# Kernel tuning notes

Measured on AMD Instinct MI355X. Metric: run time of the kernel, lower is better.

Reference implementation:

```python
import jax, jax.numpy as jnp
import numpy as np

HEADS = 4
DIM_HEAD = 32
SCALE = DIM_HEAD ** -0.5


def setup_inputs() -> dict:
    key = jax.random.key(0)
    k1, k2, k3 = jax.random.split(key, 3)
    dim, hidden = 256, HEADS * DIM_HEAD
    x = jax.random.normal(k1, (4, dim, 64, 64), dtype=jnp.float32)
    w_qkv = jax.random.normal(k2, (hidden * 3, dim), dtype=jnp.float32) * (dim ** -0.5)
    w_out = jax.random.normal(k3, (dim, hidden), dtype=jnp.float32) * (hidden ** -0.5)
    b_out = jnp.zeros((dim,), dtype=jnp.float32)
    return {"x": x, "w_qkv": w_qkv, "w_out": w_out, "b_out": b_out}


def reference(x, w_qkv, w_out, b_out):
    b, c, h, w = x.shape
    # 1x1 conv (no bias) == channel matmul
    qkv = jnp.einsum('bchw,oc->bohw', x, w_qkv)           # [b, 3*hidden, h, w]
    q, k, v = jnp.split(qkv, 3, axis=1)
    def to_heads(t):
        # [b, heads*d, h, w] -> [b, heads, h*w, d]
        return t.reshape(b, HEADS, DIM_HEAD, h * w).transpose(0, 1, 3, 2)
    q, k, v = to_heads(q) * SCALE, to_heads(k), to_heads(v)
    sim = jnp.einsum('bhid,bhjd->bhij', q, k)             # [b, heads, hw, hw]
    attn = jax.nn.softmax(sim, axis=-1)
    out = jnp.einsum('bhij,bhjd->bhid', attn, v)          # [b, heads, hw, d]
    out = out.transpose(0, 1, 3, 2).reshape(b, HEADS * DIM_HEAD, h, w)
    # output 1x1 conv with bias
    return jnp.einsum('bchw,oc->bohw', out, w_out) + b_out[None, :, None, None]
```

## Files before the change

kernel.cpp:

```cpp
#include <hip/hip_runtime.h>
#include <hip/hip_fp16.h>

#define HEADS 4
#define DH    32
#define HW    4096
#define CIN   256
#define HID   128

using half8   = __attribute__((ext_vector_type(8))) _Float16;
using half4   = __attribute__((ext_vector_type(4))) _Float16;
using floatx4 = __attribute__((ext_vector_type(4))) float;

#define SHIFT2 4.328085122666891f
#define WQSCALE 0.25508275947f

__global__ __launch_bounds__(256) void qkv_fused(
    const float* __restrict__ w, const float* __restrict__ x,
    _Float16* __restrict__ Qw, _Float16* __restrict__ Kw,
    _Float16* __restrict__ Vtw)
{
  __shared__ float t[64][65];
  __shared__ _Float16 As[64][72];
  __shared__ _Float16 Bs[64][72];
  const int mt = blockIdx.x, nt = blockIdx.y;
  const int b = nt >> 6, p0 = (nt & 63) * 64;
  const int tid = threadIdx.x;
  const int wv = tid >> 6, lane = tid & 63, lm = lane & 15, quad = lane >> 4;
  const float wscale = (mt < 2) ? WQSCALE : 1.0f;

  const float* Ag = w + (size_t)(mt * 64) * CIN;
  const float* xb = x + (size_t)b * CIN * HW + p0;

  floatx4 acc[4] = {{0,0,0,0},{0,0,0,0},{0,0,0,0},{0,0,0,0}};

  for (int kq = 0; kq < 4; ++kq) {
    __syncthreads();
    #pragma unroll
    for (int i = 0; i < 4; ++i) {
      int ci = tid + i * 256;
      int cc = ci >> 4, p4 = (ci & 15) * 4;
      *(float4*)&t[cc][p4] =
          *(const float4*)(xb + (size_t)(kq * 64 + cc) * HW + p4);
    }
    #pragma unroll
    for (int i = 0; i < 2; ++i) {
      int ci = tid + i * 256;
      int r = ci >> 3, c8 = (ci & 7) * 8;
      const float* src = Ag + (size_t)r * CIN + kq * 64 + c8;
      float4 u0 = *(const float4*)(src);
      float4 u1 = *(const float4*)(src + 4);
      half8 h = {(_Float16)(u0.x * wscale), (_Float16)(u0.y * wscale),
                 (_Float16)(u0.z * wscale), (_Float16)(u0.w * wscale),
                 (_Float16)(u1.x * wscale), (_Float16)(u1.y * wscale),
                 (_Float16)(u1.z * wscale), (_Float16)(u1.w * wscale)};
      *(half8*)&As[r][c8] = h;
    }
    __syncthreads();
    #pragma unroll
    for (int i = 0; i < 2; ++i) {
      int idx = tid + i * 256;
      int p = idx >> 3, c0 = (idx & 7) * 8;
      half8 v;
      #pragma unroll
      for (int k = 0; k < 8; ++k) v[k] = (_Float16)t[c0 + k][p];
      *(half8*)&Bs[p][c0] = v;
    }
    __syncthreads();
    #pragma unroll
    for (int ks = 0; ks < 2; ++ks) {
      half8 a = *(const half8*)&As[wv * 16 + lm][ks * 32 + quad * 8];
      #pragma unroll
      for (int ns = 0; ns < 4; ++ns) {
        half8 bf = *(const half8*)&Bs[ns * 16 + lm][ks * 32 + quad * 8];
        acc[ns] = __builtin_amdgcn_mfma_f32_16x16x32_f16(a, bf, acc[ns], 0, 0, 0);
      }
    }
  }

  const int sec = mt >> 1;
  const int o_base = (mt & 1) * 64 + wv * 16 + quad * 4;
  const int hh = o_base >> 5, dd = o_base & 31;
  const int bh = b * HEADS + hh;
  if (sec < 2) {
    _Float16* dst = (sec == 0) ? Qw : Kw;
    #pragma unroll
    for (int ns = 0; ns < 4; ++ns) {
      int p = p0 + ns * 16 + lm;
      half4 v = {(_Float16)acc[ns][0], (_Float16)acc[ns][1],
                 (_Float16)acc[ns][2], (_Float16)acc[ns][3]};
      *(half4*)(dst + ((size_t)bh * HW + p) * DH + dd) = v;
    }
  } else {
    #pragma unroll
    for (int ns = 0; ns < 4; ++ns) {
      int p = p0 + ns * 16 + lm;
      #pragma unroll
      for (int r = 0; r < 4; ++r)
        Vtw[((size_t)bh * DH + dd + r) * HW + p] = (_Float16)acc[ns][r];
    }
  }
}

__global__ __launch_bounds__(256) void attn(
    const _Float16* __restrict__ Qw, const _Float16* __restrict__ Kw,
    const _Float16* __restrict__ Vtw, _Float16* __restrict__ Ot)
{
  __shared__ _Float16 ks[2][2][64][40];
  __shared__ _Float16 vt[2][2][32][72];

  const int bh = blockIdx.y, qt = blockIdx.x;
  const int tid = threadIdx.x;
  const int wv = tid >> 6, lane = tid & 63, lm = lane & 15, quad = lane >> 4;

  const _Float16* qptr = Qw + ((size_t)bh * HW + qt * 64 + wv * 16 + lm) * DH + quad * 8;
  const half8 qa = *(const half8*)qptr;

  const _Float16 one = (_Float16)1.0f;
  const half4 ones4 = {one, one, one, one};
  const floatx4 shiftc = {-SHIFT2, -SHIFT2, -SHIFT2, -SHIFT2};

  floatx4 oT[2] = {{0,0,0,0},{0,0,0,0}};
  floatx4 l4    = {0,0,0,0};

  const _Float16* kbase = Kw  + (size_t)bh * HW * DH;
  const _Float16* vbase = Vtw + (size_t)bh * DH * HW;
  const int kr = tid >> 2, kc = (tid & 3) * 8;
  const int vr = tid >> 3, vc = (tid & 7) * 8;

  half8 kA = *(const half8*)(kbase + (size_t)kr * DH + kc);
  half8 vA = *(const half8*)(vbase + (size_t)vr * HW + vc);
  half8 kB = *(const half8*)(kbase + ((size_t)64 + kr) * DH + kc);
  half8 vB = *(const half8*)(vbase + (size_t)vr * HW + 64 + vc);
  *(half8*)&ks[0][0][kr][kc] = kA;
  *(half8*)&vt[0][0][vr][vc] = vA;
  *(half8*)&ks[0][1][kr][kc] = kB;
  *(half8*)&vt[0][1][vr][vc] = vB;
  kA = *(const half8*)(kbase + ((size_t)128 + kr) * DH + kc);
  vA = *(const half8*)(vbase + (size_t)vr * HW + 128 + vc);
  kB = *(const half8*)(kbase + ((size_t)192 + kr) * DH + kc);
  vB = *(const half8*)(vbase + (size_t)vr * HW + 192 + vc);
  __syncthreads();

  for (int it = 0; it < HW / 128; ++it) {
    const int ph = it & 1, nx = ph ^ 1;
    *(half8*)&ks[nx][0][kr][kc] = kA;
    *(half8*)&vt[nx][0][vr][vc] = vA;
    *(half8*)&ks[nx][1][kr][kc] = kB;
    *(half8*)&vt[nx][1][vr][vc] = vB;
    const size_t koff = (size_t)(it * 2 + 4) * 64;
    kA = *(const half8*)(kbase + (koff + kr) * DH + kc);
    vA = *(const half8*)(vbase + (size_t)vr * HW + koff + vc);
    kB = *(const half8*)(kbase + (koff + 64 + kr) * DH + kc);
    vB = *(const half8*)(vbase + (size_t)vr * HW + koff + 64 + vc);

    #pragma unroll
    for (int sub = 0; sub < 2; ++sub) {
      floatx4 sT[4];
      #pragma unroll
      for (int f = 0; f < 4; ++f) {
        half8 kb = *(const half8*)&ks[ph][sub][f * 16 + lm][quad * 8];
        sT[f] = __builtin_amdgcn_mfma_f32_16x16x32_f16(kb, qa, shiftc, 0, 0, 0);
      }
      #pragma unroll
      for (int f = 0; f < 4; ++f) {
        half4 pb;
        #pragma unroll
        for (int r = 0; r < 4; ++r)
          pb[r] = (_Float16)__builtin_amdgcn_exp2f(sT[f][r]);
        l4 = __builtin_amdgcn_mfma_f32_16x16x16f16(ones4, pb, l4, 0, 0, 0);
        #pragma unroll
        for (int g = 0; g < 2; ++g) {
          half4 va = *(const half4*)&vt[ph][sub][g * 16 + lm][f * 16 + quad * 4];
          oT[g] = __builtin_amdgcn_mfma_f32_16x16x16f16(va, pb, oT[g], 0, 0, 0);
        }
      }
    }
    __syncthreads();
  }

  const float inv = 1.0f / l4[0];
  const int b = bh >> 2, hh = bh & 3;
  _Float16* obase = Ot + ((size_t)(b * HW + qt * 64 + wv * 16 + lm)) * HID + hh * DH;
  #pragma unroll
  for (int g = 0; g < 2; ++g) {
    half4 v = {(_Float16)(oT[g][0] * inv), (_Float16)(oT[g][1] * inv),
               (_Float16)(oT[g][2] * inv), (_Float16)(oT[g][3] * inv)};
    *(half4*)(obase + g * 16 + quad * 4) = v;
  }
}

__global__ __launch_bounds__(256) void out_gemm(
    const float* __restrict__ wo, const _Float16* __restrict__ Ot,
    const float* __restrict__ bo, float* __restrict__ out)
{
  __shared__ _Float16 As[64][136];
  __shared__ _Float16 Bs[64][136];
  __shared__ float os[64][68];
  const int mt = blockIdx.x, nt = blockIdx.y;
  const int b = nt >> 6, p0 = (nt & 63) * 64;
  const int tid = threadIdx.x;
  const int wv = tid >> 6, lane = tid & 63, lm = lane & 15, quad = lane >> 4;

  const float* Ag = wo + (size_t)(mt * 64) * HID;
  const _Float16* B = Ot + ((size_t)b * HW + p0) * HID;

  #pragma unroll
  for (int i = 0; i < 4; ++i) {
    int ci = tid + i * 256;
    int r = ci >> 4, c8 = (ci & 15) * 8;
    const float* src = Ag + (size_t)r * HID + c8;
    float4 u0 = *(const float4*)(src);
    float4 u1 = *(const float4*)(src + 4);
    half8 h = {(_Float16)u0.x, (_Float16)u0.y, (_Float16)u0.z, (_Float16)u0.w,
               (_Float16)u1.x, (_Float16)u1.y, (_Float16)u1.z, (_Float16)u1.w};
    *(half8*)&As[r][c8] = h;
    *(half8*)&Bs[r][c8] = *(const half8*)(B + (size_t)r * HID + c8);
  }
  __syncthreads();

  floatx4 acc[4] = {{0,0,0,0},{0,0,0,0},{0,0,0,0},{0,0,0,0}};
  #pragma unroll
  for (int ks = 0; ks < 4; ++ks) {
    half8 a = *(const half8*)&As[wv * 16 + lm][ks * 32 + quad * 8];
    #pragma unroll
    for (int ns = 0; ns < 4; ++ns) {
      half8 bf = *(const half8*)&Bs[ns * 16 + lm][ks * 32 + quad * 8];
      acc[ns] = __builtin_amdgcn_mfma_f32_16x16x32_f16(a, bf, acc[ns], 0, 0, 0);
    }
  }

  #pragma unroll
  for (int ns = 0; ns < 4; ++ns)
    #pragma unroll
    for (int r = 0; r < 4; ++r)
      os[wv * 16 + quad * 4 + r][ns * 16 + lm] = acc[ns][r];
  __syncthreads();

  const int o = tid >> 2, pq = (tid & 3) * 16;
  const float bias = bo[mt * 64 + o];
  float* dst = out + ((size_t)(b * CIN + mt * 64 + o)) * HW + p0 + pq;
  #pragma unroll
  for (int j = 0; j < 4; ++j) {
    float4 v = *(const float4*)&os[o][pq + j * 4];
    v.x += bias; v.y += bias; v.z += bias; v.w += bias;
    *(float4*)(dst + j * 4) = v;
  }
}

extern "C" void kernel_launch(void* const* d_in, const int* in_sizes, int n_in,
                              void* d_out, int out_size, void* d_ws, size_t ws_size,
                              hipStream_t stream)
{
  const float* x     = (const float*)d_in[0];
  const float* w_qkv = (const float*)d_in[1];
  const float* w_out = (const float*)d_in[2];
  const float* b_out = (const float*)d_in[3];
  float* out = (float*)d_out;

  char* ws = (char*)d_ws;
  _Float16* Ot  = (_Float16*)(ws);
  _Float16* Qw  = (_Float16*)(ws + (8u  << 20));
  _Float16* Kw  = (_Float16*)(ws + (12u << 20));
  _Float16* Vtw = (_Float16*)(ws + (16u << 20));

  dim3 blk(256);
  qkv_fused<<<dim3(6, 256), blk, 0, stream>>>(w_qkv, x, Qw, Kw, Vtw);
  attn<<<dim3(64, 16), blk, 0, stream>>>(Qw, Kw, Vtw, Ot);
  out_gemm<<<dim3(4, 256), blk, 0, stream>>>(w_out, Ot, b_out, out);
}
```

Measured before the change: 165.4 us.

## Process two query tiles per attention block to reuse staged K/V tiles

```diff
diff --git a/kernel.cpp b/kernel.cpp
--- a/kernel.cpp
+++ b/kernel.cpp
@@ -9,10 +9,15 @@
 
 using half8   = __attribute__((ext_vector_type(8))) _Float16;
 using half4   = __attribute__((ext_vector_type(4))) _Float16;
+using half2v  = __attribute__((ext_vector_type(2))) _Float16;
 using floatx4 = __attribute__((ext_vector_type(4))) float;
 
 #define SHIFT2 4.328085122666891f
 #define WQSCALE 0.25508275947f
+
+static __device__ __forceinline__ half2v pk2(float a, float b) {
+  return __builtin_bit_cast(half2v, __builtin_amdgcn_cvt_pkrtz(a, b));
+}
 
 __global__ __launch_bounds__(256) void qkv_fused(
     const float* __restrict__ w, const float* __restrict__ x,
@@ -106,21 +111,23 @@
     const _Float16* __restrict__ Vtw, _Float16* __restrict__ Ot)
 {
   __shared__ _Float16 ks[2][2][64][40];
-  __shared__ _Float16 vt[2][2][32][72];
+  __shared__ _Float16 vt[2][2][32][74];
 
   const int bh = blockIdx.y, qt = blockIdx.x;
   const int tid = threadIdx.x;
   const int wv = tid >> 6, lane = tid & 63, lm = lane & 15, quad = lane >> 4;
 
-  const _Float16* qptr = Qw + ((size_t)bh * HW + qt * 64 + wv * 16 + lm) * DH + quad * 8;
-  const half8 qa = *(const half8*)qptr;
+  const _Float16* qbase =
+      Qw + ((size_t)bh * HW + qt * 128 + wv * 16 + lm) * DH + quad * 8;
+  const half8 qa0 = *(const half8*)qbase;
+  const half8 qa1 = *(const half8*)(qbase + (size_t)64 * DH);
 
   const _Float16 one = (_Float16)1.0f;
   const half4 ones4 = {one, one, one, one};
   const floatx4 shiftc = {-SHIFT2, -SHIFT2, -SHIFT2, -SHIFT2};
 
-  floatx4 oT[2] = {{0,0,0,0},{0,0,0,0}};
-  floatx4 l4    = {0,0,0,0};
+  floatx4 oT[2][2] = {{{0,0,0,0},{0,0,0,0}},{{0,0,0,0},{0,0,0,0}}};
+  floatx4 l4[2]    = {{0,0,0,0},{0,0,0,0}};
 
   const _Float16* kbase = Kw  + (size_t)bh * HW * DH;
   const _Float16* vbase = Vtw + (size_t)bh * DH * HW;
@@ -147,7 +154,8 @@
     *(half8*)&vt[nx][0][vr][vc] = vA;
     *(half8*)&ks[nx][1][kr][kc] = kB;
     *(half8*)&vt[nx][1][vr][vc] = vB;
-    const size_t koff = (size_t)(it * 2 + 4) * 64;
+    size_t koff = (size_t)(it * 2 + 4) * 64;
+    if (koff > HW - 128) koff = HW - 128;
     kA = *(const half8*)(kbase + (koff + kr) * DH + kc);
     vA = *(const half8*)(vbase + (size_t)vr * HW + koff + vc);
     kB = *(const half8*)(kbase + (koff + 64 + kr) * DH + kc);
@@ -155,37 +163,42 @@
 
     #pragma unroll
     for (int sub = 0; sub < 2; ++sub) {
-      floatx4 sT[4];
       #pragma unroll
       for (int f = 0; f < 4; ++f) {
         half8 kb = *(const half8*)&ks[ph][sub][f * 16 + lm][quad * 8];
-        sT[f] = __builtin_amdgcn_mfma_f32_16x16x32_f16(kb, qa, shiftc, 0, 0, 0);
-      }
-      #pragma unroll
-      for (int f = 0; f < 4; ++f) {
-        half4 pb;
-        #pragma unroll
-        for (int r = 0; r < 4; ++r)
-          pb[r] = (_Float16)__builtin_amdgcn_exp2f(sT[f][r]);
-        l4 = __builtin_amdgcn_mfma_f32_16x16x16f16(ones4, pb, l4, 0, 0, 0);
+        floatx4 sT0 = __builtin_amdgcn_mfma_f32_16x16x32_f16(kb, qa0, shiftc, 0, 0, 0);
+        floatx4 sT1 = __builtin_amdgcn_mfma_f32_16x16x32_f16(kb, qa1, shiftc, 0, 0, 0);
+        half2v a0 = pk2(__builtin_amdgcn_exp2f(sT0[0]), __builtin_amdgcn_exp2f(sT0[1]));
+        half2v b0 = pk2(__builtin_amdgcn_exp2f(sT0[2]), __builtin_amdgcn_exp2f(sT0[3]));
+        half2v a1 = pk2(__builtin_amdgcn_exp2f(sT1[0]), __builtin_amdgcn_exp2f(sT1[1]));
+        half2v b1 = pk2(__builtin_amdgcn_exp2f(sT1[2]), __builtin_amdgcn_exp2f(sT1[3]));
+        half4 pb0 = {a0.x, a0.y, b0.x, b0.y};
+        half4 pb1 = {a1.x, a1.y, b1.x, b1.y};
+        l4[0] = __builtin_amdgcn_mfma_f32_16x16x16f16(ones4, pb0, l4[0], 0, 0, 0);
+        l4[1] = __builtin_amdgcn_mfma_f32_16x16x16f16(ones4, pb1, l4[1], 0, 0, 0);
         #pragma unroll
         for (int g = 0; g < 2; ++g) {
           half4 va = *(const half4*)&vt[ph][sub][g * 16 + lm][f * 16 + quad * 4];
-          oT[g] = __builtin_amdgcn_mfma_f32_16x16x16f16(va, pb, oT[g], 0, 0, 0);
+          oT[0][g] = __builtin_amdgcn_mfma_f32_16x16x16f16(va, pb0, oT[0][g], 0, 0, 0);
+          oT[1][g] = __builtin_amdgcn_mfma_f32_16x16x16f16(va, pb1, oT[1][g], 0, 0, 0);
         }
       }
     }
     __syncthreads();
   }
 
-  const float inv = 1.0f / l4[0];
   const int b = bh >> 2, hh = bh & 3;
-  _Float16* obase = Ot + ((size_t)(b * HW + qt * 64 + wv * 16 + lm)) * HID + hh * DH;
-  #pragma unroll
-  for (int g = 0; g < 2; ++g) {
-    half4 v = {(_Float16)(oT[g][0] * inv), (_Float16)(oT[g][1] * inv),
-               (_Float16)(oT[g][2] * inv), (_Float16)(oT[g][3] * inv)};
-    *(half4*)(obase + g * 16 + quad * 4) = v;
+  #pragma unroll
+  for (int t = 0; t < 2; ++t) {
+    const float inv = 1.0f / l4[t][0];
+    _Float16* obase = Ot +
+        ((size_t)(b * HW + qt * 128 + t * 64 + wv * 16 + lm)) * HID + hh * DH;
+    #pragma unroll
+    for (int g = 0; g < 2; ++g) {
+      half4 v = {(_Float16)(oT[t][g][0] * inv), (_Float16)(oT[t][g][1] * inv),
+                 (_Float16)(oT[t][g][2] * inv), (_Float16)(oT[t][g][3] * inv)};
+      *(half4*)(obase + g * 16 + quad * 4) = v;
+    }
   }
 }
 
@@ -265,6 +278,6 @@
 
   dim3 blk(256);
   qkv_fused<<<dim3(6, 256), blk, 0, stream>>>(w_qkv, x, Qw, Kw, Vtw);
-  attn<<<dim3(64, 16), blk, 0, stream>>>(Qw, Kw, Vtw, Ot);
+  attn<<<dim3(32, 16), blk, 0, stream>>>(Qw, Kw, Vtw, Ot);
   out_gemm<<<dim3(4, 256), blk, 0, stream>>>(w_out, Ot, b_out, out);
 }
```

Result: no change. 165.0 us (-0.3%).
